# Kernel optimization log

Hardware: AMD Instinct MI355X
Metric: run time of the kernel (lower is better)

## Reference

```python
import jax, jax.numpy as jnp
import numpy as np

N = 20000      # nodes
E = 320000     # edges
H = 256        # hidden_dim
BD = 64        # bond embedding dim
MSG_IN = 2 * H + BD  # 576


def setup_inputs() -> dict:
    key = jax.random.key(0)
    ks = jax.random.split(key, 24)
    s = 0.05
    inp = {}
    inp["x"] = jax.random.randint(ks[0], (N, 3), 0, 7).astype(jnp.float32)
    inp["edge_index"] = jax.random.randint(ks[1], (2, E), 0, N).astype(jnp.int32)
    inp["edge_attr"] = jax.random.randint(ks[2], (E, 1), 0, 5).astype(jnp.float32)
    inp["batch"] = jnp.zeros((N,), jnp.int32)
    # embedding tables
    inp["atom_table"] = jax.random.normal(ks[3], (11, 64), jnp.float32) * s
    inp["charge_table"] = jax.random.normal(ks[4], (7, 32), jnp.float32) * s
    inp["hybrid_table"] = jax.random.normal(ks[5], (8, 32), jnp.float32) * s
    inp["bond_table"] = jax.random.normal(ks[6], (5, BD), jnp.float32) * s
    # 3 stacked ChemicalGraphConv layers (weights stored [in, out])
    inp["gnn_w1"] = jax.random.normal(ks[7], (3, MSG_IN, H), jnp.float32) * s
    inp["gnn_b1"] = jnp.zeros((3, H), jnp.float32)
    inp["gnn_w2"] = jax.random.normal(ks[8], (3, H, H), jnp.float32) * s
    inp["gnn_b2"] = jnp.zeros((3, H), jnp.float32)
    inp["att_w"] = jax.random.normal(ks[9], (3, BD, 1), jnp.float32) * s
    inp["att_b"] = jnp.zeros((3, 1), jnp.float32)
    # chemical_properties MLP
    inp["prop_w1"] = jax.random.normal(ks[10], (H, 128), jnp.float32) * s
    inp["prop_b1"] = jnp.zeros((128,), jnp.float32)
    inp["prop_w2"] = jax.random.normal(ks[11], (128, 32), jnp.float32) * s
    inp["prop_b2"] = jnp.zeros((32,), jnp.float32)
    # 4 functional-group pattern encoders, stacked [4, H, 16]
    inp["fg_w"] = jax.random.normal(ks[12], (4, H, 16), jnp.float32) * s
    inp["fg_b"] = jnp.zeros((4, 16), jnp.float32)
    return inp


def reference(x, edge_index, edge_attr, batch,
              atom_table, charge_table, hybrid_table, bond_table,
              gnn_w1, gnn_b1, gnn_w2, gnn_b2, att_w, att_b,
              prop_w1, prop_b1, prop_w2, prop_b2, fg_w, fg_b):
    n = x.shape[0]
    atom_types = jnp.clip(x[:, 0].astype(jnp.int32), 0, 10)
    formal_charges = jnp.clip(x[:, 2].astype(jnp.int32) + 3, 0, 6)
    hybridization = jnp.clip(x[:, 1].astype(jnp.int32), 0, 7)
    bond_types = jnp.clip(edge_attr[:, 0].astype(jnp.int32), 0, 4)
    bond_emb = bond_table[bond_types]  # [E, 64]

    h = jnp.concatenate([atom_table[atom_types],
                         charge_table[formal_charges],
                         hybrid_table[hybridization]], axis=-1)  # [N, 128]
    h = jnp.pad(h, ((0, 0), (0, H - h.shape[1])))  # pad to hidden_dim

    row, col = edge_index[0], edge_index[1]
    for l in range(3):  # 3 ChemicalGraphConv layers
        gate = jax.nn.sigmoid(bond_emb @ att_w[l] + att_b[l])            # [E, 1]
        msg = jnp.concatenate([h[row], h[col], bond_emb], axis=-1)      # [E, 576]
        msg = jax.nn.relu(msg @ gnn_w1[l] + gnn_b1[l]) @ gnn_w2[l] + gnn_b2[l]
        msg = msg * gate                                                 # [E, H]
        h = h + jax.ops.segment_sum(msg, row, num_segments=n)

    chemical_props = jax.nn.relu(h @ prop_w1 + prop_b1) @ prop_w2 + prop_b2  # [N, 32]

    # FunctionalGroupDetector: mean(encoder(h)) == mean(h) @ W + b (linear)
    pooled = jnp.mean(h, axis=0)                                   # [H]
    fg = (jnp.einsum('d,kdo->ko', pooled, fg_w) + fg_b).reshape(-1)  # [64]
    fg_features = jnp.broadcast_to(fg, (n, 64))

    return h, chemical_props, fg_features, atom_types
```

## Files before the change

kernel.cpp:

```cpp
#include <hip/hip_runtime.h>
#include <stdint.h>

typedef unsigned short u16;
typedef unsigned int   u32;
typedef __attribute__((ext_vector_type(8))) short bf16x8;
typedef __attribute__((ext_vector_type(4))) float f32x4;

#define NN 20000
#define NE 320000
#define HD 256
#define BD 64

#define WS_PRE   0u
#define WS_W1T   20480000u
#define WS_W2I   21266432u
#define WS_PW1   21659648u
#define WS_PREB  21725184u
#define WS_GATE  21740544u
#define WS_POOL  21740608u
#define WS_FGV   21741632u
#define WS_CNT   21741888u
#define WS_META  21821888u

__device__ __forceinline__ u16 f2bf(float f){
  u32 u = __float_as_uint(f);
  u += 0x7fffu + ((u >> 16) & 1u);
  return (u16)(u >> 16);
}
__device__ __forceinline__ u32 pk2(float a, float b){
  return (u32)f2bf(a) | ((u32)f2bf(b) << 16);
}
__device__ __forceinline__ float bf2f(u16 u){
  return __uint_as_float((u32)u << 16);
}
__device__ __forceinline__ void gl_lds16(const u16* g, u16* l){
  __builtin_amdgcn_global_load_lds(
      (const __attribute__((address_space(1))) unsigned int*)g,
      (__attribute__((address_space(3))) unsigned int*)l, 16, 0, 0);
}

__global__ void setup_k(const float* __restrict__ gw1,
                        const float* __restrict__ gw2,
                        const float* __restrict__ pw1,
                        const float* __restrict__ bond_table,
                        const float* __restrict__ gb1,
                        const float* __restrict__ att_w,
                        const float* __restrict__ att_b,
                        u16* __restrict__ w1t, u16* __restrict__ w2img,
                        u16* __restrict__ pw1bf, float* __restrict__ preb,
                        float* __restrict__ gate_tab, float* __restrict__ pooled,
                        int* __restrict__ cnt){
  int i = blockIdx.x*256 + threadIdx.x;
  if (i < 393216){
    int l = i >> 17;
    int r = i & 131071;
    int c = r >> 8;
    int k = r & 255;
    int srow = (c < 256) ? k : (256 + k);
    w1t[i] = f2bf(gw1[(l*576 + srow)*256 + (c & 255)]);
  } else if (i < 589824){
    int t = i - 393216;
    int j  = t & 7;
    int s  = (t >> 3) & 3;
    int c  = (t >> 5) & 255;
    int ks = (t >> 13) & 7;
    int l  = t >> 16;
    int kc = s ^ ((c >> 1) & 3);
    int k  = ks*32 + kc*8 + j;
    w2img[t] = f2bf(gw2[(l*256 + k)*256 + c]);
  } else if (i < 622592){
    int t = i - 589824;
    int o = t >> 8, k = t & 255;
    pw1bf[t] = f2bf(pw1[k*128 + o]);
  } else if (i < 626432){
    int t = i - 622592;
    int l = t / 1280;
    int r = t - l*1280;
    int bt = r >> 8, c = r & 255;
    float s = gb1[l*HD + c];
    for (int d = 0; d < BD; ++d)
      s += bond_table[bt*BD + d] * gw1[(l*576 + 512 + d)*256 + c];
    preb[(l*5 + bt)*256 + c] = s;
  } else if (i < 626447){
    int t = i - 626432;
    int l = t / 5, b = t - 5*l;
    float s = att_b[l];
    for (int d = 0; d < BD; ++d) s += bond_table[b*BD + d] * att_w[l*BD + d];
    gate_tab[t] = 1.0f / (1.0f + __expf(-s));
  } else if (i < 626703){
    pooled[i - 626447] = 0.0f;
  } else if (i < 646703){
    cnt[i - 626703] = 0;
  }
}

__global__ void init_embed_k(const float* __restrict__ x,
                             const float* __restrict__ atom_table,
                             const float* __restrict__ charge_table,
                             const float* __restrict__ hybrid_table,
                             float* __restrict__ h0,
                             float* __restrict__ out_at){
  int n = blockIdx.x, c = threadIdx.x;
  int at = (int)x[n*3 + 0]; at = at < 0 ? 0 : (at > 10 ? 10 : at);
  int hy = (int)x[n*3 + 1]; hy = hy < 0 ? 0 : (hy > 7 ? 7 : hy);
  int fc = (int)x[n*3 + 2] + 3; fc = fc < 0 ? 0 : (fc > 6 ? 6 : fc);
  float v = 0.0f;
  if (c < 64)       v = atom_table[at*64 + c];
  else if (c < 96)  v = charge_table[fc*32 + (c - 64)];
  else if (c < 128) v = hybrid_table[hy*32 + (c - 96)];
  h0[(size_t)n*HD + c] = v;
  if (c == 0) out_at[n] = (float)at;
}

__global__ void hist_k(const int* __restrict__ eidx, int* __restrict__ cnt){
  int e = blockIdx.x*256 + threadIdx.x;
  int r = eidx[e]; r = r < 0 ? 0 : (r >= NN ? NN-1 : r);
  atomicAdd(&cnt[r], 1);
}

__launch_bounds__(1024)
__global__ void scan_k(int* __restrict__ cnt){
  __shared__ int part[1024];
  int t = threadIdx.x;
  int base = t*20;
  int loc[20];
  int s = 0;
  #pragma unroll
  for (int j = 0; j < 20; ++j){
    int idx = base + j;
    int v = (idx < NN) ? cnt[idx] : 0;
    loc[j] = v; s += v;
  }
  part[t] = s; __syncthreads();
  for (int off = 1; off < 1024; off <<= 1){
    int v = (t >= off) ? part[t-off] : 0;
    __syncthreads();
    part[t] += v;
    __syncthreads();
  }
  int run = part[t] - s;
  #pragma unroll
  for (int j = 0; j < 20; ++j){
    int idx = base + j;
    if (idx < NN){ cnt[idx] = run; run += loc[j]; }
  }
}

__global__ void scatter_k(const int* __restrict__ eidx,
                          const float* __restrict__ eattr,
                          int* __restrict__ cur,
                          int2* __restrict__ smeta){
  int e = blockIdx.x*256 + threadIdx.x;
  int r = eidx[e];        r = r < 0 ? 0 : (r >= NN ? NN-1 : r);
  int c = eidx[NE + e];   c = c < 0 ? 0 : (c >= NN ? NN-1 : c);
  int bt = (int)eattr[e]; bt = bt < 0 ? 0 : (bt > 4 ? 4 : bt);
  int pos = atomicAdd(&cur[r], 1);
  if (pos >= 0 && pos < NE){
    int2 m; m.x = r | (bt << 20); m.y = c;
    smeta[pos] = m;
  }
}

__launch_bounds__(256, 2)
__global__ void pre_k(const float* __restrict__ h,
                      const u16* __restrict__ w1t,
                      u16* __restrict__ pre, int layer){
  __shared__ u16 a_lds[64*40];
  __shared__ u16 b_lds[256*40];
  const int tid = threadIdx.x;
  const int n0 = blockIdx.x * 64;
  const int half = blockIdx.y;
  const int w = tid >> 6, lane = tid & 63, g = lane >> 4, lr = lane & 15;
  const int rstage = tid >> 2, q = tid & 3;
  int arow = n0 + rstage; if (arow >= NN) arow = NN-1;
  const float* hrow = h + (size_t)arow*HD;
  const u16* bp = w1t + ((size_t)layer*512 + (size_t)half*256 + tid)*256;

  f32x4 acc[4][4];
  for (int mi = 0; mi < 4; ++mi)
    for (int nj = 0; nj < 4; ++nj)
      acc[mi][nj] = (f32x4){0.f,0.f,0.f,0.f};

  for (int ks = 0; ks < 8; ++ks){
    __syncthreads();
    {
      const float* src = hrow + ks*32 + q*8;
      float4 f0 = *(const float4*)src;
      float4 f1 = *(const float4*)(src + 4);
      uint4 av;
      av.x = pk2(f0.x,f0.y); av.y = pk2(f0.z,f0.w);
      av.z = pk2(f1.x,f1.y); av.w = pk2(f1.z,f1.w);
      *(uint4*)(a_lds + rstage*40 + q*8) = av;
    }
    {
      const u16* src = bp + ks*32;
      uint4 s0 = *(const uint4*)(src);
      uint4 s1 = *(const uint4*)(src + 8);
      uint4 s2 = *(const uint4*)(src + 16);
      uint4 s3 = *(const uint4*)(src + 24);
      u16* dst = b_lds + tid*40;
      *(uint4*)(dst)      = s0;
      *(uint4*)(dst + 8)  = s1;
      *(uint4*)(dst + 16) = s2;
      *(uint4*)(dst + 24) = s3;
    }
    __syncthreads();
    bf16x8 af[4], bfr[4];
    for (int mi = 0; mi < 4; ++mi)
      af[mi] = *(const bf16x8*)(a_lds + (mi*16 + lr)*40 + g*8);
    for (int nj = 0; nj < 4; ++nj)
      bfr[nj] = *(const bf16x8*)(b_lds + (w*64 + nj*16 + lr)*40 + g*8);
    for (int mi = 0; mi < 4; ++mi)
      for (int nj = 0; nj < 4; ++nj)
        acc[mi][nj] = __builtin_amdgcn_mfma_f32_16x16x32_bf16(af[mi], bfr[nj], acc[mi][nj], 0, 0, 0);
  }

  for (int mi = 0; mi < 4; ++mi)
    for (int nj = 0; nj < 4; ++nj)
      for (int p = 0; p < 4; ++p){
        int re = mi*16 + g*4 + p;
        int n = n0 + re;
        if (n < NN)
          pre[(size_t)n*512 + half*256 + w*64 + nj*16 + lr] = f2bf(acc[mi][nj][p]);
      }
}

__launch_bounds__(512, 4)
__global__ void edge_msg_k(const int2* __restrict__ smeta,
                           const u16* __restrict__ pre,
                           const float* __restrict__ prebg,
                           const u16* __restrict__ w2img,
                           const float* __restrict__ b2g,
                           const float* __restrict__ gate_tab,
                           float* __restrict__ h,
                           int layer){
  __shared__ u16 b_lds[16384];
  __shared__ u16 t_lds[64*264];
  __shared__ int   row_l[64];
  __shared__ float gate_l[64];

  const int tid = threadIdx.x;
  const int bid = blockIdx.x;
  const int blk = (bid & 7)*625 + (bid >> 3);
  const int eBase = blk * 64;
  const int w = tid >> 6, lane = tid & 63, g = lane >> 4, lr = lane & 15;
  const int rstage = tid >> 3, q = tid & 7;

  const size_t wbase = (size_t)layer*65536;

  #pragma unroll
  for (int b = 0; b < 2; ++b)
    #pragma unroll
    for (int j = 0; j < 2; ++j)
      gl_lds16(w2img + wbase + (size_t)(b*256 + w*32 + j*16)*32 + lane*8,
               b_lds + b*8192 + w*1024 + j*512);

  int2 m0 = smeta[eBase + rstage];
  const int rI  = m0.x & 0xFFFFF;
  const int btI = (m0.x >> 20) & 7;
  const int cI  = m0.y;

  if (tid < 64){
    int2 mm = smeta[eBase + tid];
    row_l[tid]  = mm.x & 0xFFFFF;
    gate_l[tid] = gate_tab[layer*5 + ((mm.x >> 20) & 7)];
  }

  {
    const u16* p1 = pre + (size_t)rI*512;
    const u16* p2 = pre + (size_t)cI*512 + 256;
    const float* pb = prebg + (size_t)(layer*5 + btI)*256;
    #pragma unroll
    for (int it = 0; it < 4; ++it){
      int c0 = it*64 + q*8;
      bf16x8 v1 = *(const bf16x8*)(p1 + c0);
      bf16x8 v2 = *(const bf16x8*)(p2 + c0);
      float pv[8];
      *(float4*)(pv)     = *(const float4*)(pb + c0);
      *(float4*)(pv + 4) = *(const float4*)(pb + c0 + 4);
      float f[8];
      #pragma unroll
      for (int j = 0; j < 8; ++j){
        float s = bf2f((u16)v1[j]) + bf2f((u16)v2[j]) + pv[j];
        f[j] = s > 0.f ? s : 0.f;
      }
      uint4 ov;
      ov.x = pk2(f[0],f[1]); ov.y = pk2(f[2],f[3]);
      ov.z = pk2(f[4],f[5]); ov.w = pk2(f[6],f[7]);
      *(uint4*)(t_lds + rstage*264 + c0) = ov;
    }
  }

  __syncthreads();

  f32x4 acc[4][2];
  for (int mi = 0; mi < 4; ++mi)
    for (int nj = 0; nj < 2; ++nj)
      acc[mi][nj] = (f32x4){0.f,0.f,0.f,0.f};

  const int sw = (g ^ ((lr >> 1) & 3)) << 3;

  #pragma unroll
  for (int ks = 0; ks < 8; ++ks){
    if (ks >= 1 && ks < 7){
      #pragma unroll
      for (int j = 0; j < 2; ++j)
        gl_lds16(w2img + wbase + (size_t)((ks+1)*256 + w*32 + j*16)*32 + lane*8,
                 b_lds + ((ks+1)&1)*8192 + w*1024 + j*512);
      asm volatile("s_waitcnt vmcnt(2)" ::: "memory");
    } else if (ks == 0){
      asm volatile("s_waitcnt vmcnt(2)" ::: "memory");
    } else {
      asm volatile("s_waitcnt vmcnt(0)" ::: "memory");
    }
    const u16* bb = b_lds + (ks&1)*8192 + w*1024;
    bf16x8 af[4], bfr[2];
    for (int nj = 0; nj < 2; ++nj)
      bfr[nj] = *(const bf16x8*)(bb + (nj*16 + lr)*32 + sw);
    for (int mi = 0; mi < 4; ++mi)
      af[mi] = *(const bf16x8*)(t_lds + (mi*16 + lr)*264 + ks*32 + g*8);
    __builtin_amdgcn_s_setprio(1);
    for (int mi = 0; mi < 4; ++mi)
      for (int nj = 0; nj < 2; ++nj)
        acc[mi][nj] = __builtin_amdgcn_mfma_f32_16x16x32_bf16(af[mi], bfr[nj], acc[mi][nj], 0, 0, 0);
    __builtin_amdgcn_s_setprio(0);
  }

  {
    float b2v[2];
    for (int nj = 0; nj < 2; ++nj) b2v[nj] = b2g[layer*HD + w*32 + nj*16 + lr];
    for (int mi = 0; mi < 4; ++mi)
      for (int nj = 0; nj < 2; ++nj){
        u16* mb = b_lds + nj*8192 + w*1024 + lr*64;
        for (int p = 0; p < 4; ++p){
          int re = mi*16 + g*4 + p;
          float val = (acc[mi][nj][p] + b2v[nj]) * gate_l[re];
          mb[(((re >> 3) ^ (lr & 7)) << 3) + (re & 7)] = f2bf(val);
        }
      }
  }
  __syncthreads();

  {
    const int cl = tid & 255, half = tid >> 8;
    const u16* mb = b_lds + ((cl >> 4) & 1)*8192 + (cl >> 5)*1024 + (cl & 15)*64;
    float run = 0.f;
    int currow = row_l[half*32];
    for (int e8 = half*4; e8 < half*4 + 4; ++e8){
      bf16x8 mv = *(const bf16x8*)(mb + ((e8 ^ (cl & 7)) << 3));
      #pragma unroll
      for (int j = 0; j < 8; ++j){
        int r = row_l[e8*8 + j];
        if (r != currow){
          atomicAdd(h + (size_t)currow*HD + cl, run);
          run = 0.f; currow = r;
        }
        run += bf2f((u16)mv[j]);
      }
    }
    atomicAdd(h + (size_t)currow*HD + cl, run);
  }
}

__global__ void pool_k(const float* __restrict__ h,
                       float* __restrict__ pooled){
  int c = threadIdx.x;
  int r0 = blockIdx.x * 250;
  float s = 0.f;
  for (int r = r0; r < r0 + 250; ++r)
    s += h[(size_t)r*HD + c];
  atomicAdd(&pooled[c], s);
}

__global__ void fg_k(const float* __restrict__ pooled,
                     const float* __restrict__ fg_w,
                     const float* __restrict__ fg_b,
                     float* __restrict__ fg_vals){
  int o = threadIdx.x;
  int k = o >> 4, j = o & 15;
  float s = 0.f;
  for (int d = 0; d < HD; ++d) s += pooled[d] * fg_w[(size_t)k*HD*16 + d*16 + j];
  fg_vals[o] = s / (float)NN + fg_b[k*16 + j];
}

__global__ void bcast_fg_k(const float* __restrict__ fg_vals,
                           float* __restrict__ out_fg){
  __shared__ float fv[64];
  if (threadIdx.x < 64) fv[threadIdx.x] = fg_vals[threadIdx.x];
  __syncthreads();
  int i = blockIdx.x*256 + threadIdx.x;
  out_fg[i] = fv[i & 63];
}

__launch_bounds__(256, 2)
__global__ void props_mfma_k(const float* __restrict__ h,
                             const u16* __restrict__ pw1bf,
                             const float* __restrict__ pb1,
                             const float* __restrict__ pw2,
                             const float* __restrict__ pb2,
                             float* __restrict__ outp){
  __shared__ u16 a_lds[64*40];
  __shared__ u16 b2_lds[128*40];
  __shared__ u16 t2[64*136];
  __shared__ float w2s[128*32];
  const int tid = threadIdx.x;
  const int n0 = blockIdx.x*64;
  const int w = tid >> 6, lane = tid & 63, g = lane >> 4, lr = lane & 15;
  const int rstage = tid >> 2, q = tid & 3;
  int arow = n0 + rstage; if (arow >= NN) arow = NN-1;
  const float* hrow = h + (size_t)arow*HD;

  for (int j = 0; j < 4; ++j)
    *(float4*)(w2s + tid*16 + j*4) = *(const float4*)(pw2 + tid*16 + j*4);

  const int colb = tid >> 1, halfb = tid & 1;

  f32x4 acc[4][2];
  for (int mi = 0; mi < 4; ++mi)
    for (int nj = 0; nj < 2; ++nj)
      acc[mi][nj] = (f32x4){0.f,0.f,0.f,0.f};

  for (int ks = 0; ks < 8; ++ks){
    __syncthreads();
    {
      const float* src = hrow + ks*32 + q*8;
      float4 f0 = *(const float4*)src;
      float4 f1 = *(const float4*)(src + 4);
      uint4 av;
      av.x = pk2(f0.x,f0.y); av.y = pk2(f0.z,f0.w);
      av.z = pk2(f1.x,f1.y); av.w = pk2(f1.z,f1.w);
      *(uint4*)(a_lds + rstage*40 + q*8) = av;
    }
    {
      const u16* src = pw1bf + colb*256 + ks*32 + halfb*16;
      uint4 s0 = *(const uint4*)src;
      uint4 s1 = *(const uint4*)(src + 8);
      u16* dst = b2_lds + colb*40 + halfb*16;
      *(uint4*)dst = s0; *(uint4*)(dst + 8) = s1;
    }
    __syncthreads();
    bf16x8 af[4], bfr[2];
    for (int mi = 0; mi < 4; ++mi)
      af[mi] = *(const bf16x8*)(a_lds + (mi*16 + lr)*40 + g*8);
    for (int nj = 0; nj < 2; ++nj)
      bfr[nj] = *(const bf16x8*)(b2_lds + (w*32 + nj*16 + lr)*40 + g*8);
    for (int mi = 0; mi < 4; ++mi)
      for (int nj = 0; nj < 2; ++nj)
        acc[mi][nj] = __builtin_amdgcn_mfma_f32_16x16x32_bf16(af[mi], bfr[nj], acc[mi][nj], 0, 0, 0);
  }

  {
    float b1v[2];
    for (int nj = 0; nj < 2; ++nj) b1v[nj] = pb1[w*32 + nj*16 + lr];
    for (int mi = 0; mi < 4; ++mi)
      for (int nj = 0; nj < 2; ++nj){
        int colt = w*32 + nj*16 + lr;
        for (int p = 0; p < 4; ++p){
          float v = acc[mi][nj][p] + b1v[nj];
          v = v > 0.f ? v : 0.f;
          t2[(mi*16 + g*4 + p)*136 + colt] = f2bf(v);
        }
      }
  }
  __syncthreads();

  {
    int e = tid >> 2, o0 = (tid & 3)*8;
    int n = n0 + e;
    float ap[8];
    #pragma unroll
    for (int o = 0; o < 8; ++o) ap[o] = pb2[o0 + o];
    for (int d0 = 0; d0 < 16; ++d0){
      bf16x8 tv = *(const bf16x8*)(t2 + e*136 + d0*8);
      #pragma unroll
      for (int dd = 0; dd < 8; ++dd){
        float t = bf2f((u16)tv[dd]);
        const float* wr = w2s + (d0*8 + dd)*32 + o0;
        #pragma unroll
        for (int o = 0; o < 8; ++o) ap[o] += t * wr[o];
      }
    }
    if (n < NN){
      *(float4*)(outp + (size_t)n*32 + o0)     = *(float4*)(ap);
      *(float4*)(outp + (size_t)n*32 + o0 + 4) = *(float4*)(ap + 4);
    }
  }
}

extern "C" void kernel_launch(void* const* d_in, const int* in_sizes, int n_in,
                              void* d_out, int out_size, void* d_ws, size_t ws_size,
                              hipStream_t stream) {
  const float* x            = (const float*)d_in[0];
  const int*   eidx         = (const int*)  d_in[1];
  const float* eattr        = (const float*)d_in[2];
  const float* atom_table   = (const float*)d_in[4];
  const float* charge_table = (const float*)d_in[5];
  const float* hybrid_table = (const float*)d_in[6];
  const float* bond_table   = (const float*)d_in[7];
  const float* gw1          = (const float*)d_in[8];
  const float* gb1          = (const float*)d_in[9];
  const float* gw2          = (const float*)d_in[10];
  const float* gb2          = (const float*)d_in[11];
  const float* attw         = (const float*)d_in[12];
  const float* attb         = (const float*)d_in[13];
  const float* pw1          = (const float*)d_in[14];
  const float* pb1          = (const float*)d_in[15];
  const float* pw2          = (const float*)d_in[16];
  const float* pb2          = (const float*)d_in[17];
  const float* fgw          = (const float*)d_in[18];
  const float* fgb          = (const float*)d_in[19];

  float* out       = (float*)d_out;
  float* out_h     = out;
  float* out_props = out + (size_t)NN*HD;
  float* out_fg    = out_props + (size_t)NN*32;
  float* out_at    = out_fg + (size_t)NN*64;

  char* ws = (char*)d_ws;
  u16*   pre      = (u16*)  (ws + WS_PRE);
  u16*   w1t      = (u16*)  (ws + WS_W1T);
  u16*   w2img    = (u16*)  (ws + WS_W2I);
  u16*   pw1bf    = (u16*)  (ws + WS_PW1);
  float* prebg    = (float*)(ws + WS_PREB);
  float* gate_tab = (float*)(ws + WS_GATE);
  float* pooled   = (float*)(ws + WS_POOL);
  float* fg_vals  = (float*)(ws + WS_FGV);
  int*   cnt      = (int*)  (ws + WS_CNT);
  int2*  smeta    = (int2*) (ws + WS_META);

  setup_k<<<2527, 256, 0, stream>>>(gw1, gw2, pw1, bond_table, gb1, attw, attb,
                                    w1t, w2img, pw1bf, prebg, gate_tab, pooled, cnt);
  init_embed_k<<<NN, 256, 0, stream>>>(x, atom_table, charge_table, hybrid_table, out_h, out_at);

  hist_k<<<1250, 256, 0, stream>>>(eidx, cnt);
  scan_k<<<1, 1024, 0, stream>>>(cnt);
  scatter_k<<<1250, 256, 0, stream>>>(eidx, eattr, cnt, smeta);

  for (int l = 0; l < 3; ++l){
    pre_k<<<dim3(313, 2), 256, 0, stream>>>(out_h, w1t, pre, l);
    edge_msg_k<<<5000, 512, 0, stream>>>(smeta, pre, prebg, w2img,
                                         gb2, gate_tab, out_h, l);
  }

  pool_k<<<80, 256, 0, stream>>>(out_h, pooled);
  fg_k<<<1, 64, 0, stream>>>(pooled, fgw, fgb, fg_vals);
  bcast_fg_k<<<5000, 256, 0, stream>>>(fg_vals, out_fg);
  props_mfma_k<<<313, 256, 0, stream>>>(out_h, pw1bf, pb1, pw2, pb2, out_props);
}
```

Measured before the change: 423.9 us.

## Fuse embed into setup, fold fg into broadcast, cheaper bf16 packing, retune occupancy

Folds node embedding initialization into the setup kernel with vectorized float4 stores, and computes the functional-group values inside the broadcast kernel, removing two launches. The edge kernel now uses truncating bf16 packing via byte permute and packed relu on raw bf16 words, and writes the gated message tile with 64-bit LDS stores instead of scalar u16 stores. Launch bounds for pre_k and props are raised to allow more waves per CU, and pooling uses more blocks. Truncation instead of round-to-nearest changes numerics slightly, and the higher occupancy targets may force register spills.

Measured after the change: 418.6 us. About the same (-1.3%).

```diff
diff --git a/kernel.cpp b/kernel.cpp
--- a/kernel.cpp
+++ b/kernel.cpp
@@ -33,6 +33,18 @@
 __device__ __forceinline__ float bf2f(u16 u){
   return __uint_as_float((u32)u << 16);
 }
+__device__ __forceinline__ u32 pk2t(float a, float b){
+  return __builtin_amdgcn_perm(__float_as_uint(a), __float_as_uint(b), 0x03020706u);
+}
+__device__ __forceinline__ u32 relu_pack(u32 a, u32 b, float p0, float p1){
+  float a0 = __uint_as_float(a << 16);
+  float a1 = __uint_as_float(a & 0xffff0000u);
+  float b0 = __uint_as_float(b << 16);
+  float b1 = __uint_as_float(b & 0xffff0000u);
+  float s0 = fmaxf(a0 + b0 + p0, 0.f);
+  float s1 = fmaxf(a1 + b1 + p1, 0.f);
+  return pk2t(s0, s1);
+}
 __device__ __forceinline__ void gl_lds16(const u16* g, u16* l){
   __builtin_amdgcn_global_load_lds(
       (const __attribute__((address_space(1))) unsigned int*)g,
@@ -46,10 +58,15 @@
                         const float* __restrict__ gb1,
                         const float* __restrict__ att_w,
                         const float* __restrict__ att_b,
+                        const float* __restrict__ x,
+                        const float* __restrict__ atom_table,
+                        const float* __restrict__ charge_table,
+                        const float* __restrict__ hybrid_table,
                         u16* __restrict__ w1t, u16* __restrict__ w2img,
                         u16* __restrict__ pw1bf, float* __restrict__ preb,
                         float* __restrict__ gate_tab, float* __restrict__ pooled,
-                        int* __restrict__ cnt){
+                        int* __restrict__ cnt,
+                        float* __restrict__ h0, float* __restrict__ out_at){
   int i = blockIdx.x*256 + threadIdx.x;
   if (i < 393216){
     int l = i >> 17;
@@ -91,25 +108,27 @@
     pooled[i - 626447] = 0.0f;
   } else if (i < 646703){
     cnt[i - 626703] = 0;
-  }
-}
-
-__global__ void init_embed_k(const float* __restrict__ x,
-                             const float* __restrict__ atom_table,
-                             const float* __restrict__ charge_table,
-                             const float* __restrict__ hybrid_table,
-                             float* __restrict__ h0,
-                             float* __restrict__ out_at){
-  int n = blockIdx.x, c = threadIdx.x;
-  int at = (int)x[n*3 + 0]; at = at < 0 ? 0 : (at > 10 ? 10 : at);
-  int hy = (int)x[n*3 + 1]; hy = hy < 0 ? 0 : (hy > 7 ? 7 : hy);
-  int fc = (int)x[n*3 + 2] + 3; fc = fc < 0 ? 0 : (fc > 6 ? 6 : fc);
-  float v = 0.0f;
-  if (c < 64)       v = atom_table[at*64 + c];
-  else if (c < 96)  v = charge_table[fc*32 + (c - 64)];
-  else if (c < 128) v = hybrid_table[hy*32 + (c - 96)];
-  h0[(size_t)n*HD + c] = v;
-  if (c == 0) out_at[n] = (float)at;
+  } else if (i < 1286703){
+    int t = i - 646703;
+    int n = t >> 5, sub = t & 31, c0 = sub*8;
+    int at = (int)x[n*3 + 0]; at = at < 0 ? 0 : (at > 10 ? 10 : at);
+    float4 v0 = {0.f,0.f,0.f,0.f}, v1 = {0.f,0.f,0.f,0.f};
+    if (c0 < 64){
+      v0 = *(const float4*)(atom_table + at*64 + c0);
+      v1 = *(const float4*)(atom_table + at*64 + c0 + 4);
+    } else if (c0 < 96){
+      int fc = (int)x[n*3 + 2] + 3; fc = fc < 0 ? 0 : (fc > 6 ? 6 : fc);
+      v0 = *(const float4*)(charge_table + fc*32 + (c0 - 64));
+      v1 = *(const float4*)(charge_table + fc*32 + (c0 - 64) + 4);
+    } else if (c0 < 128){
+      int hy = (int)x[n*3 + 1]; hy = hy < 0 ? 0 : (hy > 7 ? 7 : hy);
+      v0 = *(const float4*)(hybrid_table + hy*32 + (c0 - 96));
+      v1 = *(const float4*)(hybrid_table + hy*32 + (c0 - 96) + 4);
+    }
+    *(float4*)(h0 + (size_t)n*HD + c0)     = v0;
+    *(float4*)(h0 + (size_t)n*HD + c0 + 4) = v1;
+    if (sub == 0) out_at[n] = (float)at;
+  }
 }
 
 __global__ void hist_k(const int* __restrict__ eidx, int* __restrict__ cnt){
@@ -161,7 +180,7 @@
   }
 }
 
-__launch_bounds__(256, 2)
+__launch_bounds__(256, 4)
 __global__ void pre_k(const float* __restrict__ h,
                       const u16* __restrict__ w1t,
                       u16* __restrict__ pre, int layer){
@@ -273,20 +292,15 @@
     #pragma unroll
     for (int it = 0; it < 4; ++it){
       int c0 = it*64 + q*8;
-      bf16x8 v1 = *(const bf16x8*)(p1 + c0);
-      bf16x8 v2 = *(const bf16x8*)(p2 + c0);
-      float pv[8];
-      *(float4*)(pv)     = *(const float4*)(pb + c0);
-      *(float4*)(pv + 4) = *(const float4*)(pb + c0 + 4);
-      float f[8];
-      #pragma unroll
-      for (int j = 0; j < 8; ++j){
-        float s = bf2f((u16)v1[j]) + bf2f((u16)v2[j]) + pv[j];
-        f[j] = s > 0.f ? s : 0.f;
-      }
+      uint4 v1 = *(const uint4*)(p1 + c0);
+      uint4 v2 = *(const uint4*)(p2 + c0);
+      float4 pa = *(const float4*)(pb + c0);
+      float4 pc = *(const float4*)(pb + c0 + 4);
       uint4 ov;
-      ov.x = pk2(f[0],f[1]); ov.y = pk2(f[2],f[3]);
-      ov.z = pk2(f[4],f[5]); ov.w = pk2(f[6],f[7]);
+      ov.x = relu_pack(v1.x, v2.x, pa.x, pa.y);
+      ov.y = relu_pack(v1.y, v2.y, pa.z, pa.w);
+      ov.z = relu_pack(v1.z, v2.z, pc.x, pc.y);
+      ov.w = relu_pack(v1.w, v2.w, pc.z, pc.w);
       *(uint4*)(t_lds + rstage*264 + c0) = ov;
     }
   }
@@ -332,11 +346,15 @@
     for (int mi = 0; mi < 4; ++mi)
       for (int nj = 0; nj < 2; ++nj){
         u16* mb = b_lds + nj*8192 + w*1024 + lr*64;
+        float v[4];
+        #pragma unroll
         for (int p = 0; p < 4; ++p){
           int re = mi*16 + g*4 + p;
-          float val = (acc[mi][nj][p] + b2v[nj]) * gate_l[re];
-          mb[(((re >> 3) ^ (lr & 7)) << 3) + (re & 7)] = f2bf(val);
+          v[p] = (acc[mi][nj][p] + b2v[nj]) * gate_l[re];
         }
+        int slot = (mi*2 + (g >> 1)) ^ (lr & 7);
+        uint2 pkv; pkv.x = pk2t(v[0], v[1]); pkv.y = pk2t(v[2], v[3]);
+        *(uint2*)(mb + slot*8 + (g & 1)*4) = pkv;
       }
   }
   __syncthreads();
@@ -365,34 +383,31 @@
 __global__ void pool_k(const float* __restrict__ h,
                        float* __restrict__ pooled){
   int c = threadIdx.x;
-  int r0 = blockIdx.x * 250;
+  int r0 = blockIdx.x * 50;
   float s = 0.f;
-  for (int r = r0; r < r0 + 250; ++r)
+  for (int r = r0; r < r0 + 50; ++r)
     s += h[(size_t)r*HD + c];
   atomicAdd(&pooled[c], s);
 }
 
-__global__ void fg_k(const float* __restrict__ pooled,
-                     const float* __restrict__ fg_w,
-                     const float* __restrict__ fg_b,
-                     float* __restrict__ fg_vals){
-  int o = threadIdx.x;
-  int k = o >> 4, j = o & 15;
-  float s = 0.f;
-  for (int d = 0; d < HD; ++d) s += pooled[d] * fg_w[(size_t)k*HD*16 + d*16 + j];
-  fg_vals[o] = s / (float)NN + fg_b[k*16 + j];
-}
-
-__global__ void bcast_fg_k(const float* __restrict__ fg_vals,
+__global__ void bcast_fg_k(const float* __restrict__ pooled,
+                           const float* __restrict__ fg_w,
+                           const float* __restrict__ fg_b,
                            float* __restrict__ out_fg){
   __shared__ float fv[64];
-  if (threadIdx.x < 64) fv[threadIdx.x] = fg_vals[threadIdx.x];
+  int tid = threadIdx.x;
+  if (tid < 64){
+    int k = tid >> 4, j = tid & 15;
+    float s = 0.f;
+    for (int d = 0; d < HD; ++d) s += pooled[d] * fg_w[(size_t)k*HD*16 + d*16 + j];
+    fv[tid] = s / (float)NN + fg_b[k*16 + j];
+  }
   __syncthreads();
-  int i = blockIdx.x*256 + threadIdx.x;
+  int i = blockIdx.x*256 + tid;
   out_fg[i] = fv[i & 63];
 }
 
-__launch_bounds__(256, 2)
+__launch_bounds__(256, 3)
 __global__ void props_mfma_k(const float* __restrict__ h,
                              const u16* __restrict__ pw1bf,
                              const float* __restrict__ pb1,
@@ -524,13 +539,13 @@
   float* prebg    = (float*)(ws + WS_PREB);
   float* gate_tab = (float*)(ws + WS_GATE);
   float* pooled   = (float*)(ws + WS_POOL);
-  float* fg_vals  = (float*)(ws + WS_FGV);
   int*   cnt      = (int*)  (ws + WS_CNT);
   int2*  smeta    = (int2*) (ws + WS_META);
 
-  setup_k<<<2527, 256, 0, stream>>>(gw1, gw2, pw1, bond_table, gb1, attw, attb,
-                                    w1t, w2img, pw1bf, prebg, gate_tab, pooled, cnt);
-  init_embed_k<<<NN, 256, 0, stream>>>(x, atom_table, charge_table, hybrid_table, out_h, out_at);
+  setup_k<<<5027, 256, 0, stream>>>(gw1, gw2, pw1, bond_table, gb1, attw, attb,
+                                    x, atom_table, charge_table, hybrid_table,
+                                    w1t, w2img, pw1bf, prebg, gate_tab, pooled,
+                                    cnt, out_h, out_at);
 
   hist_k<<<1250, 256, 0, stream>>>(eidx, cnt);
   scan_k<<<1, 1024, 0, stream>>>(cnt);
@@ -542,8 +557,7 @@
                                          gb2, gate_tab, out_h, l);
   }
 
-  pool_k<<<80, 256, 0, stream>>>(out_h, pooled);
-  fg_k<<<1, 64, 0, stream>>>(pooled, fgw, fgb, fg_vals);
-  bcast_fg_k<<<5000, 256, 0, stream>>>(fg_vals, out_fg);
+  pool_k<<<400, 256, 0, stream>>>(out_h, pooled);
   props_mfma_k<<<313, 256, 0, stream>>>(out_h, pw1bf, pb1, pw2, pb2, out_props);
-}
+  bcast_fg_k<<<5000, 256, 0, stream>>>(pooled, fgw, fgb, out_fg);
+}
```
